# Kernel optimization log

Hardware: AMD Instinct MI355X
Metric: run time of the kernel (lower is better)

## Reference

```python
import jax, jax.numpy as jnp
import numpy as np

B, S, DIM, NH, HD = 2, 2048, 4096, 32, 128  # head_dim = dim // n_kv_heads
ROPE_THETA = 10000.0


def _apply_rope(xh, cos, sin):
    # xh: (B, S, H, HD); cos/sin: (S, HD//2). Llama interleaved-pair rotation
    # (view head_dim as complex pairs, multiply by e^{i*theta}).
    b, s, h, d = xh.shape
    xp = xh.reshape(b, s, h, d // 2, 2)
    x0, x1 = xp[..., 0], xp[..., 1]
    c = cos[None, :, None, :]
    sn = sin[None, :, None, :]
    o0 = x0 * c - x1 * sn
    o1 = x0 * sn + x1 * c
    return jnp.stack([o0, o1], axis=-1).reshape(b, s, h, d)


def setup_inputs() -> dict:
    key = jax.random.key(0)
    ks = jax.random.split(key, 5)
    scale = 1.0 / np.sqrt(DIM)
    x = jax.random.normal(ks[0], (B, S, DIM), dtype=jnp.float32)
    wq = jax.random.normal(ks[1], (DIM, DIM), dtype=jnp.float32) * scale
    wk = jax.random.normal(ks[2], (DIM, DIM), dtype=jnp.float32) * scale
    wv = jax.random.normal(ks[3], (DIM, DIM), dtype=jnp.float32) * scale
    wo = jax.random.normal(ks[4], (DIM, DIM), dtype=jnp.float32) * scale
    # precomputed rotary table (real/imag of freqs_cis)
    t = jnp.arange(S, dtype=jnp.float32)
    inv_freq = 1.0 / (ROPE_THETA ** (jnp.arange(0, HD, 2, dtype=jnp.float32) / HD))
    ang = t[:, None] * inv_freq[None, :]  # (S, HD//2)
    freqs_cos, freqs_sin = jnp.cos(ang), jnp.sin(ang)
    # additive causal mask
    i = jnp.arange(S)
    mask = jnp.where(i[None, :] <= i[:, None], 0.0, -jnp.inf).astype(jnp.float32)
    return {"x": x, "wq": wq, "wk": wk, "wv": wv, "wo": wo,
            "freqs_cos": freqs_cos, "freqs_sin": freqs_sin,
            "mask": mask, "start_pos": 0}


def reference(x, wq, wk, wv, wo, freqs_cos, freqs_sin, mask, start_pos):
    bsz, seqlen, dim = x.shape
    # nn.Linear(bias=False): y = x @ W^T
    xq = (x @ wq.T).reshape(bsz, seqlen, NH, HD)
    xk = (x @ wk.T).reshape(bsz, seqlen, NH, HD)
    xv = (x @ wv.T).reshape(bsz, seqlen, NH, HD)
    xq = _apply_rope(xq, freqs_cos, freqs_sin)
    xk = _apply_rope(xk, freqs_cos, freqs_sin)
    # training path: keys/values = current xk/xv (no cache)
    scores = jnp.einsum('bqhd,bkhd->bhqk', xq, xk) / np.sqrt(HD)
    scores = scores + mask[None, None, :, :]
    probs = jax.nn.softmax(scores.astype(jnp.float32), axis=-1).astype(x.dtype)
    out = jnp.einsum('bhqk,bkhd->bqhd', probs, xv).reshape(bsz, seqlen, dim)
    return out @ wo.T
```

## Files before the change

### kernel.cpp

```cpp
#include <hip/hip_runtime.h>

typedef __bf16 bf16;
typedef __attribute__((ext_vector_type(8))) __bf16 bf16x8;
typedef __attribute__((ext_vector_type(4))) float f32x4;

#define MFMA_BF16(a,b,c) __builtin_amdgcn_mfma_f32_16x16x32_bf16((a),(b),(c),0,0,0)

__device__ __forceinline__ void gld_lds16(const void* g, void* l) {
  __builtin_amdgcn_global_load_lds(
      (__attribute__((address_space(1))) void*)(g),
      (__attribute__((address_space(3))) void*)(l), 16, 0, 0);
}

__device__ __forceinline__ bf16x8 cvt8(float4 u, float4 v) {
  bf16x8 r;
  r[0] = (bf16)u.x; r[1] = (bf16)u.y; r[2] = (bf16)u.z; r[3] = (bf16)u.w;
  r[4] = (bf16)v.x; r[5] = (bf16)v.y; r[6] = (bf16)v.z; r[7] = (bf16)v.w;
  return r;
}

__global__ __launch_bounds__(256) void fill_kernel(float* p, int n, float v) {
  int i = blockIdx.x * 256 + threadIdx.x;
  if (i < n) p[i] = v;
}

__global__ __launch_bounds__(256) void cvt_kernel(const float* __restrict__ s, bf16* __restrict__ d) {
  size_t i = ((size_t)blockIdx.x * 256 + threadIdx.x) * 4;
  float4 a = *(const float4*)(s + i);
  ushort4 r;
  r.x = __builtin_bit_cast(unsigned short, (bf16)a.x);
  r.y = __builtin_bit_cast(unsigned short, (bf16)a.y);
  r.z = __builtin_bit_cast(unsigned short, (bf16)a.z);
  r.w = __builtin_bit_cast(unsigned short, (bf16)a.w);
  *(ushort4*)(d + i) = r;
}

__global__ __launch_bounds__(256) void gemm_bt_bf(
    const bf16* __restrict__ A,
    const bf16* __restrict__ W0, const bf16* __restrict__ W1, const bf16* __restrict__ W2,
    bf16* __restrict__ C0, bf16* __restrict__ C1, bf16* __restrict__ C2)
{
  constexpr int K = 4096, N = 4096;
  __shared__ __align__(16) bf16 As[128 * 32];
  __shared__ __align__(16) bf16 Bs[128 * 32];
  const int z = blockIdx.z;
  const bf16* __restrict__ W = (z == 0) ? W0 : ((z == 1) ? W1 : W2);
  bf16* __restrict__ C = (z == 0) ? C0 : ((z == 1) ? C1 : C2);
  const int tid = threadIdx.x;
  const int lane = tid & 63, wave = tid >> 6;
  const int l15 = lane & 15, quad = lane >> 4;
  const int m0 = blockIdx.x * 128, n0 = blockIdx.y * 128;
  const int wm = (wave & 1) * 64, wn = (wave >> 1) * 64;

  const int srow = tid >> 2;
  const int scol = (tid & 3) * 8;
  const bf16* gA = A + (size_t)(m0 + srow) * K + scol;
  const bf16* gW = W + (size_t)(n0 + srow) * K + scol;
  bf16* lA = &As[srow * 32 + scol];
  bf16* lB = &Bs[srow * 32 + scol];

  f32x4 acc[4][4];
#pragma unroll
  for (int i = 0; i < 4; i++)
#pragma unroll
    for (int j = 0; j < 4; j++) acc[i][j] = (f32x4){0.f, 0.f, 0.f, 0.f};

  for (int k0 = 0; k0 < K; k0 += 32) {
    __syncthreads();
    gld_lds16(gA + k0,                  lA);
    gld_lds16(gA + k0 + (size_t)64 * K, lA + 64 * 32);
    gld_lds16(gW + k0,                  lB);
    gld_lds16(gW + k0 + (size_t)64 * K, lB + 64 * 32);
    __syncthreads();
    bf16x8 af[4], bfr[4];
#pragma unroll
    for (int i = 0; i < 4; i++) af[i]  = *(const bf16x8*)&As[(wm + i * 16 + l15) * 32 + quad * 8];
#pragma unroll
    for (int j = 0; j < 4; j++) bfr[j] = *(const bf16x8*)&Bs[(wn + j * 16 + l15) * 32 + quad * 8];
#pragma unroll
    for (int i = 0; i < 4; i++)
#pragma unroll
      for (int j = 0; j < 4; j++)
        acc[i][j] = MFMA_BF16(af[i], bfr[j], acc[i][j]);
  }

  if (z == 2) {
#pragma unroll
    for (int i = 0; i < 4; i++) {
      const int mg = m0 + wm + i * 16 + quad * 4;
      const int bb = mg >> 11, ss = mg & 2047;
#pragma unroll
      for (int j = 0; j < 4; j++) {
        const int n = n0 + wn + j * 16 + l15;
        ushort4 pk;
        pk.x = __builtin_bit_cast(unsigned short, (bf16)acc[i][j][0]);
        pk.y = __builtin_bit_cast(unsigned short, (bf16)acc[i][j][1]);
        pk.z = __builtin_bit_cast(unsigned short, (bf16)acc[i][j][2]);
        pk.w = __builtin_bit_cast(unsigned short, (bf16)acc[i][j][3]);
        *(ushort4*)&C[((size_t)bb * 4096 + n) * 2048 + ss] = pk;
      }
    }
  } else {
#pragma unroll
    for (int i = 0; i < 4; i++) {
      const int row = m0 + wm + i * 16 + quad * 4;
#pragma unroll
      for (int j = 0; j < 4; j++) {
        const int col = n0 + wn + j * 16 + l15;
#pragma unroll
        for (int r = 0; r < 4; r++)
          C[(size_t)(row + r) * N + col] = (bf16)acc[i][j][r];
      }
    }
  }
}

__global__ __launch_bounds__(256) void gemm_out_bf(
    const bf16* __restrict__ A, const bf16* __restrict__ W, float* __restrict__ C)
{
  constexpr int K = 4096, N = 4096;
  __shared__ __align__(16) bf16 As[128 * 32];
  __shared__ __align__(16) bf16 Bs[128 * 32];
  const int tid = threadIdx.x;
  const int lane = tid & 63, wave = tid >> 6;
  const int l15 = lane & 15, quad = lane >> 4;
  const int m0 = blockIdx.x * 128, n0 = blockIdx.y * 128;
  const int wm = (wave & 1) * 64, wn = (wave >> 1) * 64;

  const int srow = tid >> 2;
  const int scol = (tid & 3) * 8;
  const bf16* gA = A + (size_t)(m0 + srow) * K + scol;
  const bf16* gW = W + (size_t)(n0 + srow) * K + scol;
  bf16* lA = &As[srow * 32 + scol];
  bf16* lB = &Bs[srow * 32 + scol];

  f32x4 acc[4][4];
#pragma unroll
  for (int i = 0; i < 4; i++)
#pragma unroll
    for (int j = 0; j < 4; j++) acc[i][j] = (f32x4){0.f, 0.f, 0.f, 0.f};

  for (int k0 = 0; k0 < K; k0 += 32) {
    __syncthreads();
    gld_lds16(gA + k0,                  lA);
    gld_lds16(gA + k0 + (size_t)64 * K, lA + 64 * 32);
    gld_lds16(gW + k0,                  lB);
    gld_lds16(gW + k0 + (size_t)64 * K, lB + 64 * 32);
    __syncthreads();
    bf16x8 af[4], bfr[4];
#pragma unroll
    for (int i = 0; i < 4; i++) af[i]  = *(const bf16x8*)&As[(wm + i * 16 + l15) * 32 + quad * 8];
#pragma unroll
    for (int j = 0; j < 4; j++) bfr[j] = *(const bf16x8*)&Bs[(wn + j * 16 + l15) * 32 + quad * 8];
#pragma unroll
    for (int i = 0; i < 4; i++)
#pragma unroll
      for (int j = 0; j < 4; j++)
        acc[i][j] = MFMA_BF16(af[i], bfr[j], acc[i][j]);
  }

#pragma unroll
  for (int i = 0; i < 4; i++) {
    const int row = m0 + wm + i * 16 + quad * 4;
#pragma unroll
    for (int j = 0; j < 4; j++) {
      const int col = n0 + wn + j * 16 + l15;
#pragma unroll
      for (int r = 0; r < 4; r++)
        C[(size_t)(row + r) * N + col] = acc[i][j][r];
    }
  }
}

__global__ __launch_bounds__(256) void gemm_f32in(
    const float* __restrict__ A,
    const float* __restrict__ W0, const float* __restrict__ W1, const float* __restrict__ W2,
    bf16* __restrict__ C0, bf16* __restrict__ C1, bf16* __restrict__ C2)
{
  constexpr int K = 4096, N = 4096;
  __shared__ __align__(16) bf16 As[128 * 32];
  __shared__ __align__(16) bf16 Bs[128 * 32];
  const int z = blockIdx.z;
  const float* __restrict__ W = (z == 0) ? W0 : ((z == 1) ? W1 : W2);
  bf16* __restrict__ C = (z == 0) ? C0 : ((z == 1) ? C1 : C2);
  const int tid = threadIdx.x;
  const int lane = tid & 63, wave = tid >> 6;
  const int l15 = lane & 15, quad = lane >> 4;
  const int m0 = blockIdx.x * 128, n0 = blockIdx.y * 128;
  const int wm = (wave & 1) * 64, wn = (wave >> 1) * 64;

  const int srow = tid >> 2;
  const int scol = (tid & 3) * 8;
  const float* gA = A + (size_t)(m0 + srow) * K + scol;
  const float* gW = W + (size_t)(n0 + srow) * K + scol;
  bf16* lA = &As[srow * 32 + scol];
  bf16* lB = &Bs[srow * 32 + scol];

  f32x4 acc[4][4];
#pragma unroll
  for (int i = 0; i < 4; i++)
#pragma unroll
    for (int j = 0; j < 4; j++) acc[i][j] = (f32x4){0.f, 0.f, 0.f, 0.f};

  for (int k0 = 0; k0 < K; k0 += 32) {
    float4 a0 = *(const float4*)(gA + k0);
    float4 a1 = *(const float4*)(gA + k0 + 4);
    float4 a2 = *(const float4*)(gA + k0 + (size_t)64 * K);
    float4 a3 = *(const float4*)(gA + k0 + (size_t)64 * K + 4);
    float4 b0 = *(const float4*)(gW + k0);
    float4 b1 = *(const float4*)(gW + k0 + 4);
    float4 b2 = *(const float4*)(gW + k0 + (size_t)64 * K);
    float4 b3 = *(const float4*)(gW + k0 + (size_t)64 * K + 4);
    __syncthreads();
    *(bf16x8*)lA              = cvt8(a0, a1);
    *(bf16x8*)(lA + 64 * 32)  = cvt8(a2, a3);
    *(bf16x8*)lB              = cvt8(b0, b1);
    *(bf16x8*)(lB + 64 * 32)  = cvt8(b2, b3);
    __syncthreads();
    bf16x8 af[4], bfr[4];
#pragma unroll
    for (int i = 0; i < 4; i++) af[i]  = *(const bf16x8*)&As[(wm + i * 16 + l15) * 32 + quad * 8];
#pragma unroll
    for (int j = 0; j < 4; j++) bfr[j] = *(const bf16x8*)&Bs[(wn + j * 16 + l15) * 32 + quad * 8];
#pragma unroll
    for (int i = 0; i < 4; i++)
#pragma unroll
      for (int j = 0; j < 4; j++)
        acc[i][j] = MFMA_BF16(af[i], bfr[j], acc[i][j]);
  }

  if (z == 2) {
#pragma unroll
    for (int i = 0; i < 4; i++) {
      const int mg = m0 + wm + i * 16 + quad * 4;
      const int bb = mg >> 11, ss = mg & 2047;
#pragma unroll
      for (int j = 0; j < 4; j++) {
        const int n = n0 + wn + j * 16 + l15;
        ushort4 pk;
        pk.x = __builtin_bit_cast(unsigned short, (bf16)acc[i][j][0]);
        pk.y = __builtin_bit_cast(unsigned short, (bf16)acc[i][j][1]);
        pk.z = __builtin_bit_cast(unsigned short, (bf16)acc[i][j][2]);
        pk.w = __builtin_bit_cast(unsigned short, (bf16)acc[i][j][3]);
        *(ushort4*)&C[((size_t)bb * 4096 + n) * 2048 + ss] = pk;
      }
    }
  } else {
#pragma unroll
    for (int i = 0; i < 4; i++) {
      const int row = m0 + wm + i * 16 + quad * 4;
#pragma unroll
      for (int j = 0; j < 4; j++) {
        const int col = n0 + wn + j * 16 + l15;
#pragma unroll
        for (int r = 0; r < 4; r++)
          C[(size_t)(row + r) * N + col] = (bf16)acc[i][j][r];
      }
    }
  }
}

__global__ __launch_bounds__(256) void rope_kernel(
    bf16* __restrict__ q, bf16* __restrict__ kk,
    const float* __restrict__ fc, const float* __restrict__ fs)
{
  const int t = blockIdx.x * 256 + threadIdx.x;
  const int i4 = (t & 15) << 2;
  const int row = t >> 4;
  const int s = (row >> 5) & 2047;

  float4 c4 = *(const float4*)(fc + s * 64 + i4);
  float4 s4 = *(const float4*)(fs + s * 64 + i4);
  float c[4]  = {c4.x, c4.y, c4.z, c4.w};
  float sn[4] = {s4.x, s4.y, s4.z, s4.w};

  const int off = row * 128 + (i4 << 1);
  uint4 qv = *(const uint4*)(q + off);
  uint4 kv = *(const uint4*)(kk + off);
  unsigned qa[4] = {qv.x, qv.y, qv.z, qv.w};
  unsigned ka[4] = {kv.x, kv.y, kv.z, kv.w};
#pragma unroll
  for (int p = 0; p < 4; p++) {
    float x0 = __builtin_bit_cast(float, (qa[p] & 0xffffu) << 16);
    float x1 = __builtin_bit_cast(float, (qa[p] >> 16) << 16);
    unsigned lo = __builtin_bit_cast(unsigned short, (bf16)(x0 * c[p] - x1 * sn[p]));
    unsigned hi = __builtin_bit_cast(unsigned short, (bf16)(x0 * sn[p] + x1 * c[p]));
    qa[p] = lo | (hi << 16);
    float y0 = __builtin_bit_cast(float, (ka[p] & 0xffffu) << 16);
    float y1 = __builtin_bit_cast(float, (ka[p] >> 16) << 16);
    lo = __builtin_bit_cast(unsigned short, (bf16)(y0 * c[p] - y1 * sn[p]));
    hi = __builtin_bit_cast(unsigned short, (bf16)(y0 * sn[p] + y1 * c[p]));
    ka[p] = lo | (hi << 16);
  }
  *(uint4*)(q + off)  = make_uint4(qa[0], qa[1], qa[2], qa[3]);
  *(uint4*)(kk + off) = make_uint4(ka[0], ka[1], ka[2], ka[3]);
}

__global__ __launch_bounds__(256) void flash_attn(
    const bf16* __restrict__ Kg_, const bf16* __restrict__ VT, bf16* __restrict__ QO)
{
  __shared__ __align__(16) char smem[81920];
  bf16* Qs = (bf16*)smem;
  bf16* Ks = (bf16*)(smem + 16384);
  bf16* Vs = (bf16*)(smem + 49152);

  const int tid = threadIdx.x, lane = tid & 63, wave = tid >> 6;
  const int l15 = lane & 15, quad = lane >> 4;
  const int r7 = l15 & 7;
  const int q0 = blockIdx.x * 64, h = blockIdx.y, b = blockIdx.z;

  bf16* Qg       = QO  + ((size_t)(b * 2048 + q0) * 32 + h) * 128;
  const bf16* Kg = Kg_ + ((size_t)b * 2048 * 32 + h) * 128;
  const bf16* Vg = VT  + ((size_t)(b * 32 + h)) * 128 * 2048;

#pragma unroll
  for (int it = 0; it < 4; ++it) {
    int c = it * 256 + tid;
    int rr = c >> 4, cc = (c & 15) ^ (rr & 7);
    gld_lds16(Qg + (size_t)rr * 4096 + cc * 8, &Qs[c * 8]);
  }
  __syncthreads();
  bf16x8 qf[4];
#pragma unroll
  for (int ks = 0; ks < 4; ks++)
    qf[ks] = *(const bf16x8*)&Qs[(wave * 16 + l15) * 128 + (((ks * 4 + quad) ^ r7) * 8)];

  bf16* Ps = (bf16*)smem + wave * (16 * 136);

  float m_i[4], l_i[4];
  f32x4 oacc[8];
#pragma unroll
  for (int r = 0; r < 4; r++) { m_i[r] = -INFINITY; l_i[r] = 0.f; }
#pragma unroll
  for (int j = 0; j < 8; j++) oacc[j] = (f32x4){0.f, 0.f, 0.f, 0.f};

  const float SCL = 0.08838834764831845f * 1.4426950408889634f;

  const int nct = (blockIdx.x >> 1) + 1;
  for (int ct = 0; ct < nct; ++ct) {
    __syncthreads();
    const bf16* Kt = Kg + (size_t)ct * 128 * 4096;
    const bf16* Vt = Vg + ct * 128;
#pragma unroll
    for (int it = 0; it < 8; ++it) {
      int c = it * 256 + tid;
      int rr = c >> 4, cc = (c & 15) ^ (rr & 7);
      gld_lds16(Kt + (size_t)rr * 4096 + cc * 8, &Ks[c * 8]);
      gld_lds16(Vt + (size_t)rr * 2048 + cc * 8, &Vs[c * 8]);
    }
    __syncthreads();

    f32x4 sacc[8];
#pragma unroll
    for (int nb = 0; nb < 8; nb++) {
      f32x4 a = (f32x4){0.f, 0.f, 0.f, 0.f};
#pragma unroll
      for (int ks = 0; ks < 4; ks++) {
        bf16x8 kf = *(const bf16x8*)&Ks[(nb * 16 + l15) * 128 + (((ks * 4 + quad) ^ r7) * 8)];
        a = MFMA_BF16(qf[ks], kf, a);
      }
      sacc[nb] = a;
    }

    const int qb = q0 + wave * 16 + quad * 4;
    const int kbase = ct * 128 + l15;
    float alpha[4];
#pragma unroll
    for (int r = 0; r < 4; r++) {
      float mx = -INFINITY;
#pragma unroll
      for (int nb = 0; nb < 8; nb++) {
        float s = sacc[nb][r] * SCL;
        if (kbase + nb * 16 > qb + r) s = -INFINITY;
        sacc[nb][r] = s;
        mx = fmaxf(mx, s);
      }
#pragma unroll
      for (int off = 1; off < 16; off <<= 1) mx = fmaxf(mx, __shfl_xor(mx, off));
      float mn = fmaxf(m_i[r], mx);
      alpha[r] = exp2f(m_i[r] - mn);
      m_i[r] = mn;
      float rs = 0.f;
#pragma unroll
      for (int nb = 0; nb < 8; nb++) {
        float p = exp2f(sacc[nb][r] - mn);
        rs += p;
        Ps[(quad * 4 + r) * 136 + nb * 16 + l15] = (bf16)p;
      }
#pragma unroll
      for (int off = 1; off < 16; off <<= 1) rs += __shfl_xor(rs, off);
      l_i[r] = l_i[r] * alpha[r] + rs;
    }
#pragma unroll
    for (int j = 0; j < 8; j++)
#pragma unroll
      for (int r = 0; r < 4; r++) oacc[j][r] *= alpha[r];

    __syncthreads();

#pragma unroll
    for (int ks2 = 0; ks2 < 4; ks2++) {
      bf16x8 pf = *(const bf16x8*)&Ps[l15 * 136 + ks2 * 32 + quad * 8];
#pragma unroll
      for (int j = 0; j < 8; j++) {
        bf16x8 vf = *(const bf16x8*)&Vs[(j * 16 + l15) * 128 + (((ks2 * 4 + quad) ^ r7) * 8)];
        oacc[j] = MFMA_BF16(pf, vf, oacc[j]);
      }
    }
  }

#pragma unroll
  for (int r = 0; r < 4; r++) {
    const float inv = 1.f / l_i[r];
    const int row = q0 + wave * 16 + quad * 4 + r;
    bf16* Og = QO + ((size_t)(b * 2048 + row) * 32 + h) * 128;
#pragma unroll
    for (int j = 0; j < 8; j++) Og[j * 16 + l15] = (bf16)(oacc[j][r] * inv);
  }
}

extern "C" void kernel_launch(void* const* d_in, const int* in_sizes, int n_in,
                              void* d_out, int out_size, void* d_ws, size_t ws_size,
                              hipStream_t stream) {
  const float* x  = (const float*)d_in[0];
  const float* wq = (const float*)d_in[1];
  const float* wk = (const float*)d_in[2];
  const float* wv = (const float*)d_in[3];
  const float* wo = (const float*)d_in[4];
  const float* fc = (const float*)d_in[5];
  const float* fs = (const float*)d_in[6];
  float* out = (float*)d_out;

  float sentinel = 0.f;
  if (n_in < 9 || in_sizes[0] != 16777216) sentinel = 200.f;
  else if (out_size != 16777216)           sentinel = 300.f;
  else if (in_sizes[5] != 131072)          sentinel = 400.f;
  else if (ws_size < 3ull * 33554432ull)   sentinel = 100.f;
  if (sentinel != 0.f) {
    fill_kernel<<<dim3((out_size + 255) / 256), dim3(256), 0, stream>>>(out, out_size, sentinel);
    return;
  }

  bf16* q  = (bf16*)d_ws;
  bf16* k  = q  + (size_t)16777216;
  bf16* vt = k  + (size_t)16777216;

  dim3 blk(256, 1, 1);
  const bool bigws = (ws_size >= 7ull * 33554432ull);

  if (bigws) {
    bf16* xb  = vt  + (size_t)16777216;
    bf16* wqb = xb  + (size_t)16777216;
    bf16* wkb = wqb + (size_t)16777216;
    bf16* wvb = wkb + (size_t)16777216;
    cvt_kernel<<<dim3(16384), blk, 0, stream>>>(x,  xb);
    cvt_kernel<<<dim3(16384), blk, 0, stream>>>(wq, wqb);
    cvt_kernel<<<dim3(16384), blk, 0, stream>>>(wk, wkb);
    cvt_kernel<<<dim3(16384), blk, 0, stream>>>(wv, wvb);
    gemm_bt_bf<<<dim3(32, 32, 3), blk, 0, stream>>>(xb, wqb, wkb, wvb, q, k, vt);
  } else {
    gemm_f32in<<<dim3(32, 32, 3), blk, 0, stream>>>(x, wq, wk, wv, q, k, vt);
  }
  rope_kernel<<<dim3(8192), blk, 0, stream>>>(q, k, fc, fs);
  flash_attn<<<dim3(32, 32, 2), blk, 0, stream>>>(k, vt, q);
  cvt_kernel<<<dim3(16384), blk, 0, stream>>>(wo, k);
  gemm_out_bf<<<dim3(32, 32, 1), blk, 0, stream>>>(q, k, out);
}
```

Baseline: 1.293 ms.

## Replace bf16 GEMMs with 256x256 double-buffered swizzled LDS MFMA kernel

Replaces the 128x128 single-buffered GEMM (two syncthreads per 32-wide K step) with a 256x256-tile, 512-thread kernel. It uses 128KB of double-buffered LDS with an XOR swizzle, K steps of 64, async global-to-LDS prefetch interleaved with MFMA phases, s_setprio, and a block-index swizzle for L2 locality. The aim is more data reuse per tile and hiding of global load latency behind compute in both the QKV and output projections. In exchange it needs large LDS, more registers (occupancy of one block per CU), and careful vmcnt and barrier bookkeeping.

New measurement: 1.178 ms. -8.9%, faster.

```diff
diff --git a/kernel.cpp b/kernel.cpp
--- a/kernel.cpp
+++ b/kernel.cpp
@@ -35,63 +35,129 @@
   *(ushort4*)(d + i) = r;
 }
 
-__global__ __launch_bounds__(256) void gemm_bt_bf(
+
+template<int IH, int KS>
+__device__ __forceinline__ void mfma_phase(const char* rb, int sA, int sB,
+                                           f32x4 (&acc)[8][4], bf16x8 (&bq)[4])
+{
+  bf16x8 afr[4];
+#pragma unroll
+  for (int i2 = 0; i2 < 4; ++i2)
+    afr[i2] = *(const bf16x8*)(rb + KS * 16384 + sA + (IH * 4 + i2) * 1024);
+  if (IH == 0) {
+#pragma unroll
+    for (int j = 0; j < 4; ++j)
+      bq[j] = *(const bf16x8*)(rb + 32768 + KS * 16384 + sB + j * 1024);
+  }
+  __builtin_amdgcn_s_barrier();
+  __builtin_amdgcn_s_setprio(1);
+#pragma unroll
+  for (int i2 = 0; i2 < 4; ++i2)
+#pragma unroll
+    for (int j = 0; j < 4; ++j)
+      acc[IH * 4 + i2][j] = MFMA_BF16(afr[i2], bq[j], acc[IH * 4 + i2][j]);
+  __builtin_amdgcn_s_setprio(0);
+}
+
+__device__ __forceinline__ void gemm256_core(
+    const bf16* __restrict__ Ag, const bf16* __restrict__ Wg,
+    char* smem, int m0, int n0, f32x4 (&acc)[8][4])
+{
+  constexpr int NT = 64;
+  const int tid = threadIdx.x;
+  const int lane = tid & 63;
+  const int l15 = lane & 15, quad = lane >> 4;
+  const int wave = tid >> 6;
+  const int wm = wave >> 2, wn = wave & 3;
+
+  const int swz = (((l15 & 1) * 4 + quad) ^ (l15 >> 1));
+  const int sA = ((wm * 64 + (l15 >> 1)) * 8 + swz) * 16;
+  const int sB = ((wn * 32 + (l15 >> 1)) * 8 + swz) * 16;
+
+  int r0, c0, r1, c1;
+  { int s = tid;       int rp = s >> 3, y = (s & 7) ^ (rp & 7); r0 = rp * 2 + (y >> 2); c0 = y & 3; }
+  { int s = 512 + tid; int rp = s >> 3, y = (s & 7) ^ (rp & 7); r1 = rp * 2 + (y >> 2); c1 = y & 3; }
+
+  const bf16* gA0 = Ag + (size_t)(m0 + r0) * 4096 + c0 * 8;
+  const bf16* gA1 = Ag + (size_t)(m0 + r1) * 4096 + c1 * 8;
+  const bf16* gB0 = Wg + (size_t)(n0 + r0) * 4096 + c0 * 8;
+  const bf16* gB1 = Wg + (size_t)(n0 + r1) * 4096 + c1 * 8;
+
+  const int d0 = tid * 16, d1 = (512 + tid) * 16;
+
+#pragma unroll
+  for (int i = 0; i < 8; i++)
+#pragma unroll
+    for (int j = 0; j < 4; j++) acc[i][j] = (f32x4){0.f, 0.f, 0.f, 0.f};
+
+  gld_lds16(gA0,      smem + d0);          gld_lds16(gA1,      smem + d1);
+  gld_lds16(gB0,      smem + 32768 + d0);  gld_lds16(gB1,      smem + 32768 + d1);
+  gld_lds16(gA0 + 32, smem + 16384 + d0);  gld_lds16(gA1 + 32, smem + 16384 + d1);
+  gld_lds16(gB0 + 32, smem + 49152 + d0);  gld_lds16(gB1 + 32, smem + 49152 + d1);
+
+#pragma unroll 2
+  for (int t = 0; t < NT; ++t) {
+    const int p = t & 1;
+    const char* rb = smem + p * 65536;
+    char* wb = smem + (p ^ 1) * 65536;
+    const int kn = (t + 1) * 64;
+    const bool st = (t + 1 < NT);
+
+    asm volatile("s_waitcnt vmcnt(4)" ::: "memory");
+    __builtin_amdgcn_s_barrier();
+
+    bf16x8 bq0[4];
+    if (st) { gld_lds16(gA0 + kn, wb + d0); gld_lds16(gA1 + kn, wb + d1); }
+    mfma_phase<0, 0>(rb, sA, sB, acc, bq0);
+    __builtin_amdgcn_s_barrier();
+
+    if (st) { gld_lds16(gB0 + kn, wb + 32768 + d0); gld_lds16(gB1 + kn, wb + 32768 + d1); }
+    mfma_phase<1, 0>(rb, sA, sB, acc, bq0);
+
+    if (st) asm volatile("s_waitcnt vmcnt(4)" ::: "memory");
+    else    asm volatile("s_waitcnt vmcnt(0)" ::: "memory");
+    __builtin_amdgcn_s_barrier();
+
+    bf16x8 bq1[4];
+    if (st) { gld_lds16(gA0 + kn + 32, wb + 16384 + d0); gld_lds16(gA1 + kn + 32, wb + 16384 + d1); }
+    mfma_phase<0, 1>(rb, sA, sB, acc, bq1);
+    __builtin_amdgcn_s_barrier();
+
+    if (st) { gld_lds16(gB0 + kn + 32, wb + 49152 + d0); gld_lds16(gB1 + kn + 32, wb + 49152 + d1); }
+    mfma_phase<1, 1>(rb, sA, sB, acc, bq1);
+  }
+}
+
+__global__ __launch_bounds__(512) void gemm256_qkv(
     const bf16* __restrict__ A,
     const bf16* __restrict__ W0, const bf16* __restrict__ W1, const bf16* __restrict__ W2,
     bf16* __restrict__ C0, bf16* __restrict__ C1, bf16* __restrict__ C2)
 {
-  constexpr int K = 4096, N = 4096;
-  __shared__ __align__(16) bf16 As[128 * 32];
-  __shared__ __align__(16) bf16 Bs[128 * 32];
+  __shared__ __align__(16) char smem[131072];
   const int z = blockIdx.z;
   const bf16* __restrict__ W = (z == 0) ? W0 : ((z == 1) ? W1 : W2);
   bf16* __restrict__ C = (z == 0) ? C0 : ((z == 1) ? C1 : C2);
-  const int tid = threadIdx.x;
-  const int lane = tid & 63, wave = tid >> 6;
+
+  const int bid = blockIdx.x;
+  const int swb = (bid & 7) * 32 + (bid >> 3);
+  const int m0 = (swb & 15) << 8;
+  const int n0 = (swb >> 4) << 8;
+
+  f32x4 acc[8][4];
+  gemm256_core(A, W, smem, m0, n0, acc);
+
+  const int tid = threadIdx.x, lane = tid & 63, wave = tid >> 6;
   const int l15 = lane & 15, quad = lane >> 4;
-  const int m0 = blockIdx.x * 128, n0 = blockIdx.y * 128;
-  const int wm = (wave & 1) * 64, wn = (wave >> 1) * 64;
-
-  const int srow = tid >> 2;
-  const int scol = (tid & 3) * 8;
-  const bf16* gA = A + (size_t)(m0 + srow) * K + scol;
-  const bf16* gW = W + (size_t)(n0 + srow) * K + scol;
-  bf16* lA = &As[srow * 32 + scol];
-  bf16* lB = &Bs[srow * 32 + scol];
-
-  f32x4 acc[4][4];
-#pragma unroll
-  for (int i = 0; i < 4; i++)
-#pragma unroll
-    for (int j = 0; j < 4; j++) acc[i][j] = (f32x4){0.f, 0.f, 0.f, 0.f};
-
-  for (int k0 = 0; k0 < K; k0 += 32) {
-    __syncthreads();
-    gld_lds16(gA + k0,                  lA);
-    gld_lds16(gA + k0 + (size_t)64 * K, lA + 64 * 32);
-    gld_lds16(gW + k0,                  lB);
-    gld_lds16(gW + k0 + (size_t)64 * K, lB + 64 * 32);
-    __syncthreads();
-    bf16x8 af[4], bfr[4];
-#pragma unroll
-    for (int i = 0; i < 4; i++) af[i]  = *(const bf16x8*)&As[(wm + i * 16 + l15) * 32 + quad * 8];
-#pragma unroll
-    for (int j = 0; j < 4; j++) bfr[j] = *(const bf16x8*)&Bs[(wn + j * 16 + l15) * 32 + quad * 8];
-#pragma unroll
-    for (int i = 0; i < 4; i++)
-#pragma unroll
-      for (int j = 0; j < 4; j++)
-        acc[i][j] = MFMA_BF16(af[i], bfr[j], acc[i][j]);
-  }
+  const int wm = wave >> 2, wn = wave & 3;
 
   if (z == 2) {
 #pragma unroll
-    for (int i = 0; i < 4; i++) {
-      const int mg = m0 + wm + i * 16 + quad * 4;
+    for (int i = 0; i < 8; i++) {
+      const int mg = m0 + wm * 128 + i * 16 + quad * 4;
       const int bb = mg >> 11, ss = mg & 2047;
 #pragma unroll
       for (int j = 0; j < 4; j++) {
-        const int n = n0 + wn + j * 16 + l15;
+        const int n = n0 + wn * 64 + j * 16 + l15;
         ushort4 pk;
         pk.x = __builtin_bit_cast(unsigned short, (bf16)acc[i][j][0]);
         pk.y = __builtin_bit_cast(unsigned short, (bf16)acc[i][j][1]);
@@ -102,72 +168,44 @@
     }
   } else {
 #pragma unroll
-    for (int i = 0; i < 4; i++) {
-      const int row = m0 + wm + i * 16 + quad * 4;
+    for (int i = 0; i < 8; i++) {
+      const int row = m0 + wm * 128 + i * 16 + quad * 4;
 #pragma unroll
       for (int j = 0; j < 4; j++) {
-        const int col = n0 + wn + j * 16 + l15;
+        const int col = n0 + wn * 64 + j * 16 + l15;
 #pragma unroll
         for (int r = 0; r < 4; r++)
-          C[(size_t)(row + r) * N + col] = (bf16)acc[i][j][r];
-      }
-    }
-  }
-}
-
-__global__ __launch_bounds__(256) void gemm_out_bf(
+          C[(size_t)(row + r) * 4096 + col] = (bf16)acc[i][j][r];
+      }
+    }
+  }
+}
+
+__global__ __launch_bounds__(512) void gemm256_out(
     const bf16* __restrict__ A, const bf16* __restrict__ W, float* __restrict__ C)
 {
-  constexpr int K = 4096, N = 4096;
-  __shared__ __align__(16) bf16 As[128 * 32];
-  __shared__ __align__(16) bf16 Bs[128 * 32];
-  const int tid = threadIdx.x;
-  const int lane = tid & 63, wave = tid >> 6;
+  __shared__ __align__(16) char smem[131072];
+  const int bid = blockIdx.x;
+  const int swb = (bid & 7) * 32 + (bid >> 3);
+  const int m0 = (swb & 15) << 8;
+  const int n0 = (swb >> 4) << 8;
+
+  f32x4 acc[8][4];
+  gemm256_core(A, W, smem, m0, n0, acc);
+
+  const int tid = threadIdx.x, lane = tid & 63, wave = tid >> 6;
   const int l15 = lane & 15, quad = lane >> 4;
-  const int m0 = blockIdx.x * 128, n0 = blockIdx.y * 128;
-  const int wm = (wave & 1) * 64, wn = (wave >> 1) * 64;
-
-  const int srow = tid >> 2;
-  const int scol = (tid & 3) * 8;
-  const bf16* gA = A + (size_t)(m0 + srow) * K + scol;
-  const bf16* gW = W + (size_t)(n0 + srow) * K + scol;
-  bf16* lA = &As[srow * 32 + scol];
-  bf16* lB = &Bs[srow * 32 + scol];
-
-  f32x4 acc[4][4];
-#pragma unroll
-  for (int i = 0; i < 4; i++)
-#pragma unroll
-    for (int j = 0; j < 4; j++) acc[i][j] = (f32x4){0.f, 0.f, 0.f, 0.f};
-
-  for (int k0 = 0; k0 < K; k0 += 32) {
-    __syncthreads();
-    gld_lds16(gA + k0,                  lA);
-    gld_lds16(gA + k0 + (size_t)64 * K, lA + 64 * 32);
-    gld_lds16(gW + k0,                  lB);
-    gld_lds16(gW + k0 + (size_t)64 * K, lB + 64 * 32);
-    __syncthreads();
-    bf16x8 af[4], bfr[4];
-#pragma unroll
-    for (int i = 0; i < 4; i++) af[i]  = *(const bf16x8*)&As[(wm + i * 16 + l15) * 32 + quad * 8];
-#pragma unroll
-    for (int j = 0; j < 4; j++) bfr[j] = *(const bf16x8*)&Bs[(wn + j * 16 + l15) * 32 + quad * 8];
-#pragma unroll
-    for (int i = 0; i < 4; i++)
-#pragma unroll
-      for (int j = 0; j < 4; j++)
-        acc[i][j] = MFMA_BF16(af[i], bfr[j], acc[i][j]);
-  }
-
-#pragma unroll
-  for (int i = 0; i < 4; i++) {
-    const int row = m0 + wm + i * 16 + quad * 4;
+  const int wm = wave >> 2, wn = wave & 3;
+
+#pragma unroll
+  for (int i = 0; i < 8; i++) {
+    const int row = m0 + wm * 128 + i * 16 + quad * 4;
 #pragma unroll
     for (int j = 0; j < 4; j++) {
-      const int col = n0 + wn + j * 16 + l15;
+      const int col = n0 + wn * 64 + j * 16 + l15;
 #pragma unroll
       for (int r = 0; r < 4; r++)
-        C[(size_t)(row + r) * N + col] = acc[i][j][r];
+        C[(size_t)(row + r) * 4096 + col] = acc[i][j][r];
     }
   }
 }
@@ -446,6 +484,7 @@
   bf16* vt = k  + (size_t)16777216;
 
   dim3 blk(256, 1, 1);
+  dim3 blk512(512, 1, 1);
   const bool bigws = (ws_size >= 7ull * 33554432ull);
 
   if (bigws) {
@@ -457,12 +496,12 @@
     cvt_kernel<<<dim3(16384), blk, 0, stream>>>(wq, wqb);
     cvt_kernel<<<dim3(16384), blk, 0, stream>>>(wk, wkb);
     cvt_kernel<<<dim3(16384), blk, 0, stream>>>(wv, wvb);
-    gemm_bt_bf<<<dim3(32, 32, 3), blk, 0, stream>>>(xb, wqb, wkb, wvb, q, k, vt);
+    gemm256_qkv<<<dim3(256, 1, 3), blk512, 0, stream>>>(xb, wqb, wkb, wvb, q, k, vt);
   } else {
     gemm_f32in<<<dim3(32, 32, 3), blk, 0, stream>>>(x, wq, wk, wv, q, k, vt);
   }
   rope_kernel<<<dim3(8192), blk, 0, stream>>>(q, k, fc, fs);
   flash_attn<<<dim3(32, 32, 2), blk, 0, stream>>>(k, vt, q);
   cvt_kernel<<<dim3(16384), blk, 0, stream>>>(wo, k);
-  gemm_out_bf<<<dim3(32, 32, 1), blk, 0, stream>>>(q, k, out);
-}
+  gemm256_out<<<dim3(256, 1, 1), blk512, 0, stream>>>(q, k, out);
+}
```
